# Kernel optimization log

Measured on AMD Instinct MI355X. Metric: run time of the kernel, lower is better.

The kernel has to match this reference:

```python
import jax, jax.numpy as jnp
import numpy as np

D_MODEL = 1024
N_HEADS = 16
D_K = D_MODEL // N_HEADS
D_FF = 4096
EPS = 1e-5


def setup_inputs() -> dict:
    key = jax.random.key(0)
    ks = jax.random.split(key, 16)
    s = 0.02
    d, f = D_MODEL, D_FF
    return {
        'ebd_x': jax.random.normal(ks[0], (2, 2048, d), jnp.float32),
        'Wq': jax.random.normal(ks[1], (d, d), jnp.float32) * s,
        'bq': jnp.zeros((d,), jnp.float32),
        'Wk': jax.random.normal(ks[2], (d, d), jnp.float32) * s,
        'bk': jnp.zeros((d,), jnp.float32),
        'Wv': jax.random.normal(ks[3], (d, d), jnp.float32) * s,
        'bv': jnp.zeros((d,), jnp.float32),
        'Wo': jax.random.normal(ks[4], (d, d), jnp.float32) * s,
        'bo': jnp.zeros((d,), jnp.float32),
        'W1': jax.random.normal(ks[5], (d, f), jnp.float32) * s,
        'b1': jnp.zeros((f,), jnp.float32),
        'W2': jax.random.normal(ks[6], (f, d), jnp.float32) * s,
        'b2': jnp.zeros((d,), jnp.float32),
        'g1': jnp.ones((d,), jnp.float32),
        'beta1': jnp.zeros((d,), jnp.float32),
        'g2': jnp.ones((d,), jnp.float32),
        'beta2': jnp.zeros((d,), jnp.float32),
    }


def _layernorm(x, g, b):
    mu = jnp.mean(x, axis=-1, keepdims=True)
    var = jnp.mean(jnp.square(x - mu), axis=-1, keepdims=True)
    return (x - mu) * jax.lax.rsqrt(var + EPS) * g + b


def reference(ebd_x, Wq, bq, Wk, bk, Wv, bv, Wo, bo, W1, b1, W2, b2, g1, beta1, g2, beta2):
    b, L, d = ebd_x.shape
    h, dk = N_HEADS, D_K
    # QKV projections, split heads: (b, h, L, dk)
    q = (ebd_x @ Wq + bq).reshape(b, L, h, dk).transpose(0, 2, 1, 3)
    k = (ebd_x @ Wk + bk).reshape(b, L, h, dk).transpose(0, 2, 1, 3)
    v = (ebd_x @ Wv + bv).reshape(b, L, h, dk).transpose(0, 2, 1, 3)
    scores = jnp.einsum('bhLd,bhld->bhLl', q, k) / jnp.sqrt(jnp.float32(dk))
    attn = jax.nn.softmax(scores, axis=-1)
    attn_v = jnp.einsum('bhLl,bhld->bhLd', attn, v)
    # faithful to source: reshape (b,h,L,dk) -> (b,L,d) WITHOUT transposing back
    attn_v = attn_v.reshape(b, L, d)
    attn_v = attn_v @ Wo + bo
    # dropout is identity in eval mode
    x1 = _layernorm(attn_v + ebd_x, g1, beta1)
    ff = jax.nn.gelu(x1 @ W1 + b1, approximate=False) @ W2 + b2
    return _layernorm(ff + x1, g2, beta2)
```

## Files before the change

kernel.cpp:

```cpp
#include <hip/hip_runtime.h>
#include <hip/hip_bf16.h>
#include <math.h>

typedef __bf16 bhalf;
typedef __bf16 bhalf8 __attribute__((ext_vector_type(8)));
typedef float  floatx4 __attribute__((ext_vector_type(4)));
typedef float  floatx8 __attribute__((ext_vector_type(8)));
typedef unsigned short ushort_t;
typedef unsigned short ushort8 __attribute__((ext_vector_type(8)));

#define MFMA16(a, b, c) __builtin_amdgcn_mfma_f32_16x16x32_bf16((a), (b), (c), 0, 0, 0)

__device__ __forceinline__ void gload_lds16(const bhalf* g, bhalf* l)
{
    __builtin_amdgcn_global_load_lds((const __attribute__((address_space(1))) void*)g,
                                     (__attribute__((address_space(3))) void*)l, 16, 0, 0);
}

enum { EPI_PLAIN = 0, EPI_RES = 1, EPI_GELU = 2, EPI_QKV = 3 };

__global__ __launch_bounds__(256) void detect_dtype(const ushort_t* __restrict__ x,
                                                    int* __restrict__ flag)
{
    __shared__ int tot;
    if (threadIdx.x == 0) tot = 0;
    __syncthreads();
    int cnt = 0;
#pragma unroll
    for (int it = 0; it < 8; ++it) {
        const ushort8 u = *(const ushort8*)(x + ((size_t)(it * 256 + threadIdx.x)) * 8);
#pragma unroll
        for (int j = 0; j < 8; j += 2) {
            const int e = (u[j] >> 7) & 0xFF;
            if (e >= 0x90) ++cnt;
        }
    }
    atomicAdd(&tot, cnt);
    __syncthreads();
    if (threadIdx.x == 0) flag[0] = (tot > 64) ? 1 : 0;
}

__global__ __launch_bounds__(256) void norm_x(const void* __restrict__ s,
                                              bhalf* __restrict__ d,
                                              const int* __restrict__ flag)
{
    const int i = (blockIdx.x * 256 + threadIdx.x) * 8;
    if (*flag) {
        const floatx8 v = *(const floatx8*)((const float*)s + i);
        bhalf8 o;
#pragma unroll
        for (int j = 0; j < 8; ++j) o[j] = (bhalf)v[j];
        *(bhalf8*)(d + i) = o;
    } else {
        *(ushort8*)((ushort_t*)d + i) = *(const ushort8*)((const ushort_t*)s + i);
    }
}

struct Cvt { const void* s; bhalf* d; int n; };
struct CvtArr { Cvt t[10]; };

__global__ __launch_bounds__(256) void norm_vec(CvtArr a, const int* __restrict__ flag)
{
    const Cvt c = a.t[blockIdx.y];
    const int i = (blockIdx.x * 256 + threadIdx.x) * 8;
    if (i >= c.n) return;
    if (*flag) {
        const floatx8 v = *(const floatx8*)((const float*)c.s + i);
        bhalf8 o;
#pragma unroll
        for (int j = 0; j < 8; ++j) o[j] = (bhalf)v[j];
        *(bhalf8*)(c.d + i) = o;
    } else {
        *(ushort8*)((ushort_t*)c.d + i) = *(const ushort8*)((const ushort_t*)c.s + i);
    }
}

struct TDesc { const void* src; bhalf* dst; int R, C; };
struct TDescArr { TDesc t[6]; };

__global__ __launch_bounds__(256) void transpose_all(TDescArr a, const int* __restrict__ flag)
{
    __shared__ bhalf sm[32][33];
    const int id = blockIdx.x;
    TDesc d;
    int rem;
    if (id < 4096)      { d = a.t[id >> 10]; rem = id & 1023; }
    else if (id < 8192) { d = a.t[4];        rem = id - 4096; }
    else                { d = a.t[5];        rem = id - 8192; }
    const int txc = d.C >> 5;
    const int bx = (rem % txc) * 32;
    const int by = (rem / txc) * 32;
    const int tx = threadIdx.x & 31;
    const int ty = threadIdx.x >> 5;
    if (*flag) {
        const float* fin = (const float*)d.src;
#pragma unroll
        for (int i = 0; i < 4; ++i)
            sm[ty + i * 8][tx] = (bhalf)fin[(size_t)(by + ty + i * 8) * d.C + bx + tx];
    } else {
        const bhalf* bin = (const bhalf*)d.src;
#pragma unroll
        for (int i = 0; i < 4; ++i)
            sm[ty + i * 8][tx] = bin[(size_t)(by + ty + i * 8) * d.C + bx + tx];
    }
    __syncthreads();
#pragma unroll
    for (int i = 0; i < 4; ++i)
        d.dst[(size_t)(bx + ty + i * 8) * d.R + by + tx] = sm[tx][ty + i * 8];
}

__global__ __launch_bounds__(256) void vt_transpose(const bhalf* __restrict__ Vw,
                                                    bhalf* __restrict__ Vt)
{
    __shared__ bhalf sm[32][33];
    const int bh = blockIdx.z;
    const int b = bh >> 4, h = bh & 15;
    const int tb = blockIdx.y * 32;
    const int db = blockIdx.x * 32;
    const int tx = threadIdx.x & 31;
    const int ty = threadIdx.x >> 5;
#pragma unroll
    for (int i = 0; i < 4; ++i)
        sm[ty + i * 8][tx] = Vw[(size_t)(b * 2048 + tb + ty + i * 8) * 1024 + h * 64 + db + tx];
    __syncthreads();
#pragma unroll
    for (int i = 0; i < 4; ++i)
        Vt[(size_t)(bh * 64 + db + ty + i * 8) * 2048 + tb + tx] = sm[tx][ty + i * 8];
}

template <int EPI, int TN>
__global__ __launch_bounds__(256) void gemm128(
    const bhalf* __restrict__ A, int lda,
    const bhalf* __restrict__ BT, int ldb,
    const bhalf* __restrict__ bias,
    const bhalf* __restrict__ resid,
    bhalf* __restrict__ C, int ldc, int K,
    bhalf* __restrict__ Ck, bhalf* __restrict__ Cv)
{
    __shared__ __align__(16) bhalf As[128 * 64];
    __shared__ __align__(16) bhalf Bs[TN * 64];

    const int tid  = threadIdx.x;
    const int lane = tid & 63;
    const int w    = tid >> 6;
    const int l15  = lane & 15;
    const int q    = lane >> 4;
    constexpr int MT = (TN == 128) ? 4 : 2;
    const int wm   = (TN == 128) ? (w >> 1) * 64 : w * 32;
    const int wn   = (TN == 128) ? (w & 1) * 64 : 0;
    const int n0   = blockIdx.x * TN;
    const int m0   = blockIdx.y * 128;

    const int r8 = lane >> 3;
    const int c8 = lane & 7;
    const int gc = (c8 ^ r8) << 3;

    floatx4 acc[MT][4];
#pragma unroll
    for (int i = 0; i < MT; ++i)
#pragma unroll
        for (int j = 0; j < 4; ++j) acc[i][j] = (floatx4){0.f, 0.f, 0.f, 0.f};

    for (int k0 = 0; k0 < K; k0 += 64) {
        __syncthreads();
#pragma unroll
        for (int i = 0; i < 4; ++i) {
            const int rb = w * 32 + i * 8;
            gload_lds16(A + (size_t)(m0 + rb + r8) * lda + k0 + gc, &As[rb * 64] + lane * 8);
        }
        if constexpr (TN == 128) {
#pragma unroll
            for (int i = 0; i < 4; ++i) {
                const int rb = w * 32 + i * 8;
                gload_lds16(BT + (size_t)(n0 + rb + r8) * ldb + k0 + gc, &Bs[rb * 64] + lane * 8);
            }
        } else {
#pragma unroll
            for (int i = 0; i < 2; ++i) {
                const int rb = w * 16 + i * 8;
                gload_lds16(BT + (size_t)(n0 + rb + r8) * ldb + k0 + gc, &Bs[rb * 64] + lane * 8);
            }
        }
        __syncthreads();
#pragma unroll
        for (int s = 0; s < 2; ++s) {
            const int pc = (((s * 4 + q) ^ (l15 & 7)) << 3);
            bhalf8 af[MT], bf[4];
#pragma unroll
            for (int mt = 0; mt < MT; ++mt)
                af[mt] = *(const bhalf8*)&As[(wm + mt * 16 + l15) * 64 + pc];
#pragma unroll
            for (int nt = 0; nt < 4; ++nt)
                bf[nt] = *(const bhalf8*)&Bs[(wn + nt * 16 + l15) * 64 + pc];
#pragma unroll
            for (int mt = 0; mt < MT; ++mt)
#pragma unroll
                for (int nt = 0; nt < 4; ++nt)
                    acc[mt][nt] = MFMA16(af[mt], bf[nt], acc[mt][nt]);
        }
    }

#pragma unroll
    for (int mt = 0; mt < MT; ++mt)
#pragma unroll
        for (int nt = 0; nt < 4; ++nt) {
            const int col = n0 + wn + nt * 16 + l15;
            const float bv = (float)bias[col];
#pragma unroll
            for (int r = 0; r < 4; ++r) {
                const int row = m0 + wm + mt * 16 + q * 4 + r;
                float v = acc[mt][nt][r] + bv;
                if constexpr (EPI == EPI_PLAIN) {
                    C[(size_t)row * ldc + col] = (bhalf)v;
                } else if constexpr (EPI == EPI_RES) {
                    v += (float)resid[(size_t)row * ldc + col];
                    C[(size_t)row * ldc + col] = (bhalf)v;
                } else if constexpr (EPI == EPI_GELU) {
                    v = 0.5f * v * (1.f + erff(v * 0.70710678118654752f));
                    C[(size_t)row * ldc + col] = (bhalf)v;
                } else {
                    if (col < 1024)       C [(size_t)row * 1024 + col]        = (bhalf)v;
                    else if (col < 2048)  Ck[(size_t)row * 1024 + col - 1024] = (bhalf)v;
                    else                  Cv[(size_t)row * 1024 + col - 2048] = (bhalf)v;
                }
            }
        }
}

__global__ __launch_bounds__(256) void flash_attn(
    const bhalf* __restrict__ Q, const bhalf* __restrict__ Km,
    const bhalf* __restrict__ Vt, bhalf* __restrict__ ctx)
{
    __shared__ __align__(16) bhalf Ks[2][64 * 64];
    __shared__ __align__(16) bhalf Vs[2][64 * 64];

    const int tid  = threadIdx.x;
    const int lane = tid & 63;
    const int wq   = tid >> 6;
    const int l15  = lane & 15;
    const int q    = lane >> 4;
    const int bh   = blockIdx.x & 31;
    const int l0   = (blockIdx.x >> 5) * 64;
    const int b    = bh >> 4, h = bh & 15;
    const float SC = 0.125f * 1.44269504f;

    const bhalf* qp = Q + ((size_t)(b * 2048 + l0 + wq * 16 + l15)) * 1024 + h * 64 + q * 8;
    const bhalf8 aQ0 = *(const bhalf8*)qp;
    const bhalf8 aQ1 = *(const bhalf8*)(qp + 32);

    float ps = 0.f;
    floatx4 o[4];
#pragma unroll
    for (int ot = 0; ot < 4; ++ot) o[ot] = (floatx4){0.f, 0.f, 0.f, 0.f};

    const int r8 = lane >> 3;
    const int c8 = lane & 7;
    const bhalf* kbase = Km + ((size_t)(b * 2048)) * 1024 + h * 64;
    const bhalf* vbase = Vt + ((size_t)(bh * 64)) * 2048;

    auto stage = [&](int buf, int kt) {
#pragma unroll
        for (int i = 0; i < 2; ++i) {
            const int rb = wq * 16 + i * 8;
            const int fk = (((rb >> 3) << 1) ^ r8) & 7;
            gload_lds16(kbase + (size_t)(kt + rb + r8) * 1024 + ((c8 ^ fk) << 3),
                        &Ks[buf][rb * 64] + lane * 8);
            gload_lds16(vbase + (size_t)(rb + r8) * 2048 + kt + ((c8 ^ r8) << 3),
                        &Vs[buf][rb * 64] + lane * 8);
        }
    };

    stage(0, 0);
    int cur = 0;
    for (int kt = 0; kt < 2048; kt += 64) {
        __syncthreads();
        if (kt + 64 < 2048) stage(cur ^ 1, kt + 64);

        floatx4 s[4];
#pragma unroll
        for (int nt = 0; nt < 4; ++nt) {
            const int row = (nt >> 1) * 32 + (nt & 1) * 4 + ((l15 >> 2) << 3) + (l15 & 3);
            const int f = (((row >> 3) << 1) ^ row) & 7;
            const bhalf8 k0 = *(const bhalf8*)&Ks[cur][row * 64 + ((q ^ f) << 3)];
            const bhalf8 k1 = *(const bhalf8*)&Ks[cur][row * 64 + (((4 + q) ^ f) << 3)];
            floatx4 z = (floatx4){0.f, 0.f, 0.f, 0.f};
            z = MFMA16(k0, aQ0, z);
            s[nt] = MFMA16(k1, aQ1, z);
        }

        bhalf8 pa[2];
#pragma unroll
        for (int nt = 0; nt < 4; ++nt)
#pragma unroll
            for (int r = 0; r < 4; ++r) {
                const float pv = __builtin_amdgcn_exp2f(fmaf(s[nt][r], SC, -8.f));
                ps += pv;
                pa[nt >> 1][(nt & 1) * 4 + r] = (bhalf)pv;
            }

#pragma unroll
        for (int kc = 0; kc < 2; ++kc)
#pragma unroll
            for (int ot = 0; ot < 4; ++ot) {
                const bhalf8 bV = *(const bhalf8*)&Vs[cur][(ot * 16 + l15) * 64 + (((kc * 4 + q) ^ (l15 & 7)) << 3)];
                o[ot] = MFMA16(pa[kc], bV, o[ot]);
            }
        cur ^= 1;
    }

    ps += __shfl_xor(ps, 16);
    ps += __shfl_xor(ps, 32);
    const float invq = 1.f / ps;
    float inv[4];
#pragma unroll
    for (int r = 0; r < 4; ++r)
        inv[r] = __shfl(invq, (lane & 48) | (q * 4 + r));

#pragma unroll
    for (int ot = 0; ot < 4; ++ot)
#pragma unroll
        for (int r = 0; r < 4; ++r) {
            const int l = l0 + wq * 16 + q * 4 + r;
            const int kk = ot * 16 + l15;
            const int R = h * 128 + (l >> 4);
            const int Cc = (l & 15) * 64 + kk;
            ctx[((size_t)(b * 2048 + R)) * 1024 + Cc] = (bhalf)(o[ot][r] * inv[r]);
        }
}

__global__ __launch_bounds__(256) void ln_kernel(
    const bhalf* __restrict__ X, const bhalf* __restrict__ g,
    const bhalf* __restrict__ be, void* __restrict__ out, const int* __restrict__ flag)
{
    __shared__ float red[4][2];
    const int tid = threadIdx.x;
    const int wid = tid >> 6;
    const int rid = tid >> 7;
    const int lt  = tid & 127;
    const int row = blockIdx.x * 2 + rid;
    const int col = lt * 8;
    const bhalf8 xv = *(const bhalf8*)(X + (size_t)row * 1024 + col);
    float v[8], s1 = 0.f, s2 = 0.f;
#pragma unroll
    for (int i = 0; i < 8; ++i) {
        v[i] = (float)xv[i];
        s1 += v[i];
        s2 += v[i] * v[i];
    }
#pragma unroll
    for (int off = 1; off < 64; off <<= 1) {
        s1 += __shfl_xor(s1, off);
        s2 += __shfl_xor(s2, off);
    }
    if ((tid & 63) == 0) { red[wid][0] = s1; red[wid][1] = s2; }
    __syncthreads();
    const float t1 = red[rid * 2][0] + red[rid * 2 + 1][0];
    const float t2 = red[rid * 2][1] + red[rid * 2 + 1][1];
    const float mu = t1 * (1.f / 1024.f);
    const float rs = rsqrtf(t2 * (1.f / 1024.f) - mu * mu + 1e-5f);
    const bool f32 = flag && (*flag != 0);
    if (f32) {
        floatx8 ov;
#pragma unroll
        for (int i = 0; i < 8; ++i)
            ov[i] = ((v[i] - mu) * rs) * (float)g[col + i] + (float)be[col + i];
        *(floatx8*)((float*)out + (size_t)row * 1024 + col) = ov;
    } else {
        bhalf8 ov;
#pragma unroll
        for (int i = 0; i < 8; ++i)
            ov[i] = (bhalf)(((v[i] - mu) * rs) * (float)g[col + i] + (float)be[col + i]);
        *(bhalf8*)((bhalf*)out + (size_t)row * 1024 + col) = ov;
    }
}

extern "C" void kernel_launch(void* const* d_in, const int* in_sizes, int n_in,
                              void* d_out, int out_size, void* d_ws, size_t ws_size,
                              hipStream_t stream)
{
    (void)in_sizes; (void)n_in; (void)out_size; (void)ws_size;

    char* p = (char*)d_ws;
    const size_t MB = 1024 * 1024;
    int*   flag  = (int*)p;
    bhalf* vecs  = (bhalf*)(p + 128 * 1024);
    bhalf* Qw    = (bhalf*)(p + 1 * MB);
    bhalf* Kw    = (bhalf*)(p + 9 * MB);
    bhalf* Vw    = (bhalf*)(p + 17 * MB);
    bhalf* Vt    = (bhalf*)(p + 25 * MB);
    bhalf* x_n   = (bhalf*)(p + 33 * MB);
    bhalf* WqkvT = (bhalf*)(p + 41 * MB);
    bhalf* WoT   = (bhalf*)(p + 47 * MB);
    bhalf* W1T   = (bhalf*)(p + 49 * MB);
    bhalf* W2T   = (bhalf*)(p + 57 * MB);
    bhalf* ctx   = Vw;
    bhalf* ff1   = (bhalf*)(p + 17 * MB);
    bhalf* ln1   = Qw;
    bhalf* x1    = Kw;
    bhalf* ff2   = Qw;

    bhalf* bqkv  = vecs;
    bhalf* bo_n  = vecs + 1 * 4096;
    bhalf* b1_n  = vecs + 2 * 4096;
    bhalf* b2_n  = vecs + 3 * 4096;
    bhalf* g1_n  = vecs + 4 * 4096;
    bhalf* be1_n = vecs + 5 * 4096;
    bhalf* g2_n  = vecs + 6 * 4096;
    bhalf* be2_n = vecs + 7 * 4096;

    const dim3 blk(256);

    detect_dtype<<<1, blk, 0, stream>>>((const ushort_t*)d_in[0], flag);

    norm_x<<<2048, blk, 0, stream>>>(d_in[0], x_n, flag);
    CvtArr arr;
    arr.t[0] = {d_in[2],  bqkv,        1024};
    arr.t[1] = {d_in[4],  bqkv + 1024, 1024};
    arr.t[2] = {d_in[6],  bqkv + 2048, 1024};
    arr.t[3] = {d_in[8],  bo_n,        1024};
    arr.t[4] = {d_in[10], b1_n,        4096};
    arr.t[5] = {d_in[12], b2_n,        1024};
    arr.t[6] = {d_in[13], g1_n,        1024};
    arr.t[7] = {d_in[14], be1_n,       1024};
    arr.t[8] = {d_in[15], g2_n,        1024};
    arr.t[9] = {d_in[16], be2_n,       1024};
    norm_vec<<<dim3(2, 10), blk, 0, stream>>>(arr, flag);

    TDescArr td;
    td.t[0] = {d_in[1],  WqkvT,               1024, 1024};
    td.t[1] = {d_in[3],  WqkvT + 1024 * 1024, 1024, 1024};
    td.t[2] = {d_in[5],  WqkvT + 2048 * 1024, 1024, 1024};
    td.t[3] = {d_in[7],  WoT,                 1024, 1024};
    td.t[4] = {d_in[9],  W1T,                 1024, 4096};
    td.t[5] = {d_in[11], W2T,                 4096, 1024};
    transpose_all<<<12288, blk, 0, stream>>>(td, flag);

    gemm128<EPI_QKV, 128><<<dim3(24, 32), blk, 0, stream>>>(
        x_n, 1024, WqkvT, 1024, bqkv, nullptr, Qw, 1024, 1024, Kw, Vw);

    vt_transpose<<<dim3(2, 64, 32), blk, 0, stream>>>(Vw, Vt);

    flash_attn<<<1024, blk, 0, stream>>>(Qw, Kw, Vt, ctx);

    gemm128<EPI_RES, 64><<<dim3(16, 32), blk, 0, stream>>>(
        ctx, 1024, WoT, 1024, bo_n, x_n, ln1, 1024, 1024, nullptr, nullptr);
    ln_kernel<<<2048, blk, 0, stream>>>(ln1, g1_n, be1_n, x1, nullptr);

    gemm128<EPI_GELU, 128><<<dim3(32, 32), blk, 0, stream>>>(
        x1, 1024, W1T, 1024, b1_n, nullptr, ff1, 4096, 1024, nullptr, nullptr);
    gemm128<EPI_RES, 64><<<dim3(16, 32), blk, 0, stream>>>(
        ff1, 4096, W2T, 4096, b2_n, x1, ff2, 1024, 4096, nullptr, nullptr);
    ln_kernel<<<2048, blk, 0, stream>>>(ff2, g2_n, be2_n, d_out, flag);
}
```

Before: 381.8 us.

## Add 256x256-tile GEMM with XCD-aware block mapping for QKV and FF1

Introduces a 512-thread GEMM kernel with 256x256 output tiles, double-buffered 128KB dynamic LDS loaded via global_load_lds with XOR swizzle. Block IDs are remapped across the 8 XCDs. The kernel is used for the QKV projection and the GELU FFN up-projection, replacing the 128-tile kernel. Larger tiles raise arithmetic intensity and operand reuse, but the grid shrinks to 192/256 blocks, which risks poor occupancy and load balance on 256 CUs.

```diff
diff --git a/kernel.cpp b/kernel.cpp
--- a/kernel.cpp
+++ b/kernel.cpp
@@ -222,6 +222,109 @@
                     if (col < 1024)       C [(size_t)row * 1024 + col]        = (bhalf)v;
                     else if (col < 2048)  Ck[(size_t)row * 1024 + col - 1024] = (bhalf)v;
                     else                  Cv[(size_t)row * 1024 + col - 2048] = (bhalf)v;
+                }
+            }
+        }
+}
+
+template <int EPI>
+__global__ __launch_bounds__(512, 2) void gemm256(
+    const bhalf* __restrict__ A, int lda,
+    const bhalf* __restrict__ BT, int ldb,
+    const bhalf* __restrict__ bias,
+    bhalf* __restrict__ C, int ldc, int K, int nbx,
+    bhalf* __restrict__ Ck, bhalf* __restrict__ Cv)
+{
+    extern __shared__ __align__(16) bhalf sm[];
+
+    const int tid  = threadIdx.x;
+    const int lane = tid & 63;
+    const int w    = tid >> 6;
+    const int l15  = lane & 15;
+    const int q    = lane >> 4;
+    const int wm   = (w >> 2) * 128;
+    const int wn   = (w & 3) * 64;
+    const int w8   = w * 8;
+
+    const int nwg = gridDim.x;
+    const int cpx = nwg >> 3;
+    const int id  = (blockIdx.x & 7) * cpx + (blockIdx.x >> 3);
+    const int bx  = id % nbx;
+    const int by  = id / nbx;
+    const int n0  = bx * 256;
+    const int m0  = by * 256;
+
+    const int r8 = lane >> 3;
+    const int c8 = lane & 7;
+    const int gc = (c8 ^ r8) << 3;
+
+    floatx4 acc[8][4];
+#pragma unroll
+    for (int i = 0; i < 8; ++i)
+#pragma unroll
+        for (int j = 0; j < 4; ++j) acc[i][j] = (floatx4){0.f, 0.f, 0.f, 0.f};
+
+    auto stage = [&](int buf, int k0) {
+        bhalf* as = sm + buf * 16384;
+        bhalf* bs = sm + 32768 + buf * 16384;
+#pragma unroll
+        for (int i = 0; i < 4; ++i) {
+            const int rb = i * 64 + w8;
+            gload_lds16(A  + (size_t)(m0 + rb + r8) * lda + k0 + gc, as + rb * 64 + lane * 8);
+            gload_lds16(BT + (size_t)(n0 + rb + r8) * ldb + k0 + gc, bs + rb * 64 + lane * 8);
+        }
+    };
+
+    stage(0, 0);
+    const int NT = K >> 6;
+    for (int t = 0; t < NT; ++t) {
+        const int cur = t & 1;
+        const bhalf* as = sm + cur * 16384;
+        const bhalf* bs = sm + 32768 + cur * 16384;
+        __syncthreads();
+        if (t + 1 < NT) stage(cur ^ 1, (t + 1) << 6);
+
+#pragma unroll
+        for (int ks = 0; ks < 2; ++ks) {
+            const int pc = ((ks * 4 + q) ^ (l15 & 7)) << 3;
+            bhalf8 bf[4];
+#pragma unroll
+            for (int nt = 0; nt < 4; ++nt)
+                bf[nt] = *(const bhalf8*)&bs[(wn + nt * 16 + l15) * 64 + pc];
+#pragma unroll
+            for (int mh = 0; mh < 2; ++mh) {
+                bhalf8 af[4];
+#pragma unroll
+                for (int mt = 0; mt < 4; ++mt)
+                    af[mt] = *(const bhalf8*)&as[(wm + mh * 64 + mt * 16 + l15) * 64 + pc];
+#pragma unroll
+                for (int mt = 0; mt < 4; ++mt)
+#pragma unroll
+                    for (int nt = 0; nt < 4; ++nt)
+                        acc[mh * 4 + mt][nt] = MFMA16(af[mt], bf[nt], acc[mh * 4 + mt][nt]);
+            }
+        }
+    }
+
+#pragma unroll
+    for (int j = 0; j < 8; ++j)
+#pragma unroll
+        for (int nt = 0; nt < 4; ++nt) {
+            const int col = n0 + wn + nt * 16 + l15;
+            const float bv = (float)bias[col];
+#pragma unroll
+            for (int r = 0; r < 4; ++r) {
+                const int row = m0 + wm + (j >> 2) * 64 + (j & 3) * 16 + q * 4 + r;
+                float v = acc[j][nt][r] + bv;
+                if constexpr (EPI == EPI_GELU) {
+                    v = 0.5f * v * (1.f + erff(v * 0.70710678118654752f));
+                    C[(size_t)row * ldc + col] = (bhalf)v;
+                } else if constexpr (EPI == EPI_QKV) {
+                    if (col < 1024)       C [(size_t)row * 1024 + col]        = (bhalf)v;
+                    else if (col < 2048)  Ck[(size_t)row * 1024 + col - 1024] = (bhalf)v;
+                    else                  Cv[(size_t)row * 1024 + col - 2048] = (bhalf)v;
+                } else {
+                    C[(size_t)row * ldc + col] = (bhalf)v;
                 }
             }
         }
@@ -408,7 +511,17 @@
     bhalf* g2_n  = vecs + 6 * 4096;
     bhalf* be2_n = vecs + 7 * 4096;
 
+    static bool attr_done = false;
+    if (!attr_done) {
+        hipFuncSetAttribute((const void*)gemm256<EPI_QKV>,
+                            hipFuncAttributeMaxDynamicSharedMemorySize, 131072);
+        hipFuncSetAttribute((const void*)gemm256<EPI_GELU>,
+                            hipFuncAttributeMaxDynamicSharedMemorySize, 131072);
+        attr_done = true;
+    }
+
     const dim3 blk(256);
+    const dim3 blk512(512);
 
     detect_dtype<<<1, blk, 0, stream>>>((const ushort_t*)d_in[0], flag);
 
@@ -435,8 +548,8 @@
     td.t[5] = {d_in[11], W2T,                 4096, 1024};
     transpose_all<<<12288, blk, 0, stream>>>(td, flag);
 
-    gemm128<EPI_QKV, 128><<<dim3(24, 32), blk, 0, stream>>>(
-        x_n, 1024, WqkvT, 1024, bqkv, nullptr, Qw, 1024, 1024, Kw, Vw);
+    gemm256<EPI_QKV><<<192, blk512, 131072, stream>>>(
+        x_n, 1024, WqkvT, 1024, bqkv, Qw, 1024, 1024, 12, Kw, Vw);
 
     vt_transpose<<<dim3(2, 64, 32), blk, 0, stream>>>(Vw, Vt);
 
@@ -446,8 +559,8 @@
         ctx, 1024, WoT, 1024, bo_n, x_n, ln1, 1024, 1024, nullptr, nullptr);
     ln_kernel<<<2048, blk, 0, stream>>>(ln1, g1_n, be1_n, x1, nullptr);
 
-    gemm128<EPI_GELU, 128><<<dim3(32, 32), blk, 0, stream>>>(
-        x1, 1024, W1T, 1024, b1_n, nullptr, ff1, 4096, 1024, nullptr, nullptr);
+    gemm256<EPI_GELU><<<256, blk512, 131072, stream>>>(
+        x1, 1024, W1T, 1024, b1_n, ff1, 4096, 1024, 16, nullptr, nullptr);
     gemm128<EPI_RES, 64><<<dim3(16, 32), blk, 0, stream>>>(
         ff1, 4096, W2T, 4096, b2_n, x1, ff2, 1024, 4096, nullptr, nullptr);
     ln_kernel<<<2048, blk, 0, stream>>>(ff2, g2_n, be2_n, d_out, flag);
```

New measurement: 369.9 us. 3.1% less time.

## Double-buffer GEMM LDS tiles, unify 128x64 tiles, remap blocks across XCDs

Applied to the files above, without the earlier changes.

The GEMM kernel now uses double-buffered LDS, prefetching the next K tile with global_load_lds while MFMAs consume the current one. This removes one barrier per iteration. All GEMMs now use a single 128x64 tile shape on a 1D grid. Block IDs are remapped so that consecutive tiles land on the same XCD (blockIdx mod 8 grouping), which is meant to improve L2 reuse. The 64-wide N tile lowers per-block arithmetic intensity for the QKV and W1 GEMMs and doubles the LDS footprint, which could hurt occupancy.

```diff
diff --git a/kernel.cpp b/kernel.cpp
--- a/kernel.cpp
+++ b/kernel.cpp
@@ -128,72 +128,73 @@
         Vt[(size_t)(bh * 64 + db + ty + i * 8) * 2048 + tb + tx] = sm[tx][ty + i * 8];
 }
 
-template <int EPI, int TN>
+template <int EPI>
 __global__ __launch_bounds__(256) void gemm128(
     const bhalf* __restrict__ A, int lda,
     const bhalf* __restrict__ BT, int ldb,
     const bhalf* __restrict__ bias,
     const bhalf* __restrict__ resid,
-    bhalf* __restrict__ C, int ldc, int K,
+    bhalf* __restrict__ C, int ldc, int K, int nbx,
     bhalf* __restrict__ Ck, bhalf* __restrict__ Cv)
 {
-    __shared__ __align__(16) bhalf As[128 * 64];
-    __shared__ __align__(16) bhalf Bs[TN * 64];
+    __shared__ __align__(16) bhalf As[2][128 * 64];
+    __shared__ __align__(16) bhalf Bs[2][64 * 64];
 
     const int tid  = threadIdx.x;
     const int lane = tid & 63;
     const int w    = tid >> 6;
     const int l15  = lane & 15;
     const int q    = lane >> 4;
-    constexpr int MT = (TN == 128) ? 4 : 2;
-    const int wm   = (TN == 128) ? (w >> 1) * 64 : w * 32;
-    const int wn   = (TN == 128) ? (w & 1) * 64 : 0;
-    const int n0   = blockIdx.x * TN;
-    const int m0   = blockIdx.y * 128;
+    const int wm   = w * 32;
+
+    const int nwg = gridDim.x;
+    const int cpx = nwg >> 3;
+    const int id  = (blockIdx.x & 7) * cpx + (blockIdx.x >> 3);
+    const int n0  = (id % nbx) * 64;
+    const int m0  = (id / nbx) * 128;
 
     const int r8 = lane >> 3;
     const int c8 = lane & 7;
     const int gc = (c8 ^ r8) << 3;
 
-    floatx4 acc[MT][4];
-#pragma unroll
-    for (int i = 0; i < MT; ++i)
+    floatx4 acc[2][4];
+#pragma unroll
+    for (int i = 0; i < 2; ++i)
 #pragma unroll
         for (int j = 0; j < 4; ++j) acc[i][j] = (floatx4){0.f, 0.f, 0.f, 0.f};
 
-    for (int k0 = 0; k0 < K; k0 += 64) {
-        __syncthreads();
+    auto stage = [&](int buf, int k0) {
 #pragma unroll
         for (int i = 0; i < 4; ++i) {
             const int rb = w * 32 + i * 8;
-            gload_lds16(A + (size_t)(m0 + rb + r8) * lda + k0 + gc, &As[rb * 64] + lane * 8);
-        }
-        if constexpr (TN == 128) {
-#pragma unroll
-            for (int i = 0; i < 4; ++i) {
-                const int rb = w * 32 + i * 8;
-                gload_lds16(BT + (size_t)(n0 + rb + r8) * ldb + k0 + gc, &Bs[rb * 64] + lane * 8);
-            }
-        } else {
-#pragma unroll
-            for (int i = 0; i < 2; ++i) {
-                const int rb = w * 16 + i * 8;
-                gload_lds16(BT + (size_t)(n0 + rb + r8) * ldb + k0 + gc, &Bs[rb * 64] + lane * 8);
-            }
-        }
+            gload_lds16(A + (size_t)(m0 + rb + r8) * lda + k0 + gc, &As[buf][rb * 64] + lane * 8);
+        }
+#pragma unroll
+        for (int i = 0; i < 2; ++i) {
+            const int rb = w * 16 + i * 8;
+            gload_lds16(BT + (size_t)(n0 + rb + r8) * ldb + k0 + gc, &Bs[buf][rb * 64] + lane * 8);
+        }
+    };
+
+    stage(0, 0);
+    const int NT = K >> 6;
+    for (int t = 0; t < NT; ++t) {
+        const int cur = t & 1;
         __syncthreads();
+        if (t + 1 < NT) stage(cur ^ 1, (t + 1) << 6);
+
 #pragma unroll
         for (int s = 0; s < 2; ++s) {
             const int pc = (((s * 4 + q) ^ (l15 & 7)) << 3);
-            bhalf8 af[MT], bf[4];
-#pragma unroll
-            for (int mt = 0; mt < MT; ++mt)
-                af[mt] = *(const bhalf8*)&As[(wm + mt * 16 + l15) * 64 + pc];
+            bhalf8 af[2], bf[4];
+#pragma unroll
+            for (int mt = 0; mt < 2; ++mt)
+                af[mt] = *(const bhalf8*)&As[cur][(wm + mt * 16 + l15) * 64 + pc];
 #pragma unroll
             for (int nt = 0; nt < 4; ++nt)
-                bf[nt] = *(const bhalf8*)&Bs[(wn + nt * 16 + l15) * 64 + pc];
-#pragma unroll
-            for (int mt = 0; mt < MT; ++mt)
+                bf[nt] = *(const bhalf8*)&Bs[cur][(nt * 16 + l15) * 64 + pc];
+#pragma unroll
+            for (int mt = 0; mt < 2; ++mt)
 #pragma unroll
                 for (int nt = 0; nt < 4; ++nt)
                     acc[mt][nt] = MFMA16(af[mt], bf[nt], acc[mt][nt]);
@@ -201,27 +202,27 @@
     }
 
 #pragma unroll
-    for (int mt = 0; mt < MT; ++mt)
+    for (int mt = 0; mt < 2; ++mt)
 #pragma unroll
         for (int nt = 0; nt < 4; ++nt) {
-            const int col = n0 + wn + nt * 16 + l15;
+            const int col = n0 + nt * 16 + l15;
             const float bv = (float)bias[col];
 #pragma unroll
             for (int r = 0; r < 4; ++r) {
                 const int row = m0 + wm + mt * 16 + q * 4 + r;
                 float v = acc[mt][nt][r] + bv;
-                if constexpr (EPI == EPI_PLAIN) {
-                    C[(size_t)row * ldc + col] = (bhalf)v;
-                } else if constexpr (EPI == EPI_RES) {
+                if constexpr (EPI == EPI_RES) {
                     v += (float)resid[(size_t)row * ldc + col];
                     C[(size_t)row * ldc + col] = (bhalf)v;
                 } else if constexpr (EPI == EPI_GELU) {
                     v = 0.5f * v * (1.f + erff(v * 0.70710678118654752f));
                     C[(size_t)row * ldc + col] = (bhalf)v;
-                } else {
+                } else if constexpr (EPI == EPI_QKV) {
                     if (col < 1024)       C [(size_t)row * 1024 + col]        = (bhalf)v;
                     else if (col < 2048)  Ck[(size_t)row * 1024 + col - 1024] = (bhalf)v;
                     else                  Cv[(size_t)row * 1024 + col - 2048] = (bhalf)v;
+                } else {
+                    C[(size_t)row * ldc + col] = (bhalf)v;
                 }
             }
         }
@@ -435,20 +436,20 @@
     td.t[5] = {d_in[11], W2T,                 4096, 1024};
     transpose_all<<<12288, blk, 0, stream>>>(td, flag);
 
-    gemm128<EPI_QKV, 128><<<dim3(24, 32), blk, 0, stream>>>(
-        x_n, 1024, WqkvT, 1024, bqkv, nullptr, Qw, 1024, 1024, Kw, Vw);
+    gemm128<EPI_QKV><<<1536, blk, 0, stream>>>(
+        x_n, 1024, WqkvT, 1024, bqkv, nullptr, Qw, 1024, 1024, 48, Kw, Vw);
 
     vt_transpose<<<dim3(2, 64, 32), blk, 0, stream>>>(Vw, Vt);
 
     flash_attn<<<1024, blk, 0, stream>>>(Qw, Kw, Vt, ctx);
 
-    gemm128<EPI_RES, 64><<<dim3(16, 32), blk, 0, stream>>>(
-        ctx, 1024, WoT, 1024, bo_n, x_n, ln1, 1024, 1024, nullptr, nullptr);
+    gemm128<EPI_RES><<<512, blk, 0, stream>>>(
+        ctx, 1024, WoT, 1024, bo_n, x_n, ln1, 1024, 1024, 16, nullptr, nullptr);
     ln_kernel<<<2048, blk, 0, stream>>>(ln1, g1_n, be1_n, x1, nullptr);
 
-    gemm128<EPI_GELU, 128><<<dim3(32, 32), blk, 0, stream>>>(
-        x1, 1024, W1T, 1024, b1_n, nullptr, ff1, 4096, 1024, nullptr, nullptr);
-    gemm128<EPI_RES, 64><<<dim3(16, 32), blk, 0, stream>>>(
-        ff1, 4096, W2T, 4096, b2_n, x1, ff2, 1024, 4096, nullptr, nullptr);
+    gemm128<EPI_GELU><<<2048, blk, 0, stream>>>(
+        x1, 1024, W1T, 1024, b1_n, nullptr, ff1, 4096, 1024, 64, nullptr, nullptr);
+    gemm128<EPI_RES><<<512, blk, 0, stream>>>(
+        ff1, 4096, W2T, 4096, b2_n, x1, ff2, 1024, 4096, 16, nullptr, nullptr);
     ln_kernel<<<2048, blk, 0, stream>>>(ff2, g2_n, be2_n, d_out, flag);
 }
```

Measured after the change: 380.2 us. No clear change (-0.4%).

## Double-buffer GEMM LDS tiles and remap workgroups across XCDs

Applied to the files above, without the earlier changes.

The GEMM kernel now keeps two LDS buffers per operand and issues the global-to-LDS loads for the next K tile before computing the current one, so load latency overlaps with MFMA work. The launch grid is flattened to 1D and workgroup IDs are permuted so that neighbouring tiles land on the same XCD, which should improve L2 reuse of A/B panels. This doubles LDS usage per block, which may reduce occupancy. The loop also assumes an even number of K tiles.

```diff
diff --git a/kernel.cpp b/kernel.cpp
--- a/kernel.cpp
+++ b/kernel.cpp
@@ -134,22 +134,26 @@
     const bhalf* __restrict__ BT, int ldb,
     const bhalf* __restrict__ bias,
     const bhalf* __restrict__ resid,
-    bhalf* __restrict__ C, int ldc, int K,
+    bhalf* __restrict__ C, int ldc, int K, int nbx,
     bhalf* __restrict__ Ck, bhalf* __restrict__ Cv)
 {
-    __shared__ __align__(16) bhalf As[128 * 64];
-    __shared__ __align__(16) bhalf Bs[TN * 64];
+    constexpr int MT = (TN == 128) ? 4 : 2;
+    __shared__ __align__(16) bhalf As[2][128 * 64];
+    __shared__ __align__(16) bhalf Bs[2][TN * 64];
 
     const int tid  = threadIdx.x;
     const int lane = tid & 63;
     const int w    = tid >> 6;
     const int l15  = lane & 15;
     const int q    = lane >> 4;
-    constexpr int MT = (TN == 128) ? 4 : 2;
     const int wm   = (TN == 128) ? (w >> 1) * 64 : w * 32;
     const int wn   = (TN == 128) ? (w & 1) * 64 : 0;
-    const int n0   = blockIdx.x * TN;
-    const int m0   = blockIdx.y * 128;
+
+    const int nwg = gridDim.x;
+    const int cpx = nwg >> 3;
+    const int id  = (blockIdx.x & 7) * cpx + (blockIdx.x >> 3);
+    const int n0  = (id % nbx) * TN;
+    const int m0  = (id / nbx) * 128;
 
     const int r8 = lane >> 3;
     const int c8 = lane & 7;
@@ -161,43 +165,58 @@
 #pragma unroll
         for (int j = 0; j < 4; ++j) acc[i][j] = (floatx4){0.f, 0.f, 0.f, 0.f};
 
-    for (int k0 = 0; k0 < K; k0 += 64) {
-        __syncthreads();
+    const bhalf* Ab = A  + (size_t)(m0 + r8) * lda + gc;
+    const bhalf* Bb = BT + (size_t)(n0 + r8) * ldb + gc;
+
+    auto stage = [&](int buf, int k0) {
 #pragma unroll
         for (int i = 0; i < 4; ++i) {
             const int rb = w * 32 + i * 8;
-            gload_lds16(A + (size_t)(m0 + rb + r8) * lda + k0 + gc, &As[rb * 64] + lane * 8);
+            gload_lds16(Ab + (size_t)rb * lda + k0, &As[buf][rb * 64] + lane * 8);
         }
         if constexpr (TN == 128) {
 #pragma unroll
             for (int i = 0; i < 4; ++i) {
                 const int rb = w * 32 + i * 8;
-                gload_lds16(BT + (size_t)(n0 + rb + r8) * ldb + k0 + gc, &Bs[rb * 64] + lane * 8);
+                gload_lds16(Bb + (size_t)rb * ldb + k0, &Bs[buf][rb * 64] + lane * 8);
             }
         } else {
 #pragma unroll
             for (int i = 0; i < 2; ++i) {
                 const int rb = w * 16 + i * 8;
-                gload_lds16(BT + (size_t)(n0 + rb + r8) * ldb + k0 + gc, &Bs[rb * 64] + lane * 8);
+                gload_lds16(Bb + (size_t)rb * ldb + k0, &Bs[buf][rb * 64] + lane * 8);
             }
         }
-        __syncthreads();
+    };
+
+    auto compute = [&](int buf) {
 #pragma unroll
         for (int s = 0; s < 2; ++s) {
             const int pc = (((s * 4 + q) ^ (l15 & 7)) << 3);
             bhalf8 af[MT], bf[4];
 #pragma unroll
             for (int mt = 0; mt < MT; ++mt)
-                af[mt] = *(const bhalf8*)&As[(wm + mt * 16 + l15) * 64 + pc];
+                af[mt] = *(const bhalf8*)&As[buf][(wm + mt * 16 + l15) * 64 + pc];
 #pragma unroll
             for (int nt = 0; nt < 4; ++nt)
-                bf[nt] = *(const bhalf8*)&Bs[(wn + nt * 16 + l15) * 64 + pc];
+                bf[nt] = *(const bhalf8*)&Bs[buf][(wn + nt * 16 + l15) * 64 + pc];
 #pragma unroll
             for (int mt = 0; mt < MT; ++mt)
 #pragma unroll
                 for (int nt = 0; nt < 4; ++nt)
                     acc[mt][nt] = MFMA16(af[mt], bf[nt], acc[mt][nt]);
         }
+    };
+
+    stage(0, 0);
+    const int NT = K >> 6;
+    for (int t = 0; t < NT; t += 2) {
+        __syncthreads();
+        stage(1, (t + 1) << 6);
+        compute(0);
+        __syncthreads();
+        if (t + 2 < NT) stage(0, (t + 2) << 6);
+        compute(1);
     }
 
 #pragma unroll
@@ -210,18 +229,18 @@
             for (int r = 0; r < 4; ++r) {
                 const int row = m0 + wm + mt * 16 + q * 4 + r;
                 float v = acc[mt][nt][r] + bv;
-                if constexpr (EPI == EPI_PLAIN) {
-                    C[(size_t)row * ldc + col] = (bhalf)v;
-                } else if constexpr (EPI == EPI_RES) {
+                if constexpr (EPI == EPI_RES) {
                     v += (float)resid[(size_t)row * ldc + col];
                     C[(size_t)row * ldc + col] = (bhalf)v;
                 } else if constexpr (EPI == EPI_GELU) {
                     v = 0.5f * v * (1.f + erff(v * 0.70710678118654752f));
                     C[(size_t)row * ldc + col] = (bhalf)v;
-                } else {
+                } else if constexpr (EPI == EPI_QKV) {
                     if (col < 1024)       C [(size_t)row * 1024 + col]        = (bhalf)v;
                     else if (col < 2048)  Ck[(size_t)row * 1024 + col - 1024] = (bhalf)v;
                     else                  Cv[(size_t)row * 1024 + col - 2048] = (bhalf)v;
+                } else {
+                    C[(size_t)row * ldc + col] = (bhalf)v;
                 }
             }
         }
@@ -435,20 +454,20 @@
     td.t[5] = {d_in[11], W2T,                 4096, 1024};
     transpose_all<<<12288, blk, 0, stream>>>(td, flag);
 
-    gemm128<EPI_QKV, 128><<<dim3(24, 32), blk, 0, stream>>>(
-        x_n, 1024, WqkvT, 1024, bqkv, nullptr, Qw, 1024, 1024, Kw, Vw);
+    gemm128<EPI_QKV, 128><<<768, blk, 0, stream>>>(
+        x_n, 1024, WqkvT, 1024, bqkv, nullptr, Qw, 1024, 1024, 24, Kw, Vw);
 
     vt_transpose<<<dim3(2, 64, 32), blk, 0, stream>>>(Vw, Vt);
 
     flash_attn<<<1024, blk, 0, stream>>>(Qw, Kw, Vt, ctx);
 
-    gemm128<EPI_RES, 64><<<dim3(16, 32), blk, 0, stream>>>(
-        ctx, 1024, WoT, 1024, bo_n, x_n, ln1, 1024, 1024, nullptr, nullptr);
+    gemm128<EPI_RES, 64><<<512, blk, 0, stream>>>(
+        ctx, 1024, WoT, 1024, bo_n, x_n, ln1, 1024, 1024, 16, nullptr, nullptr);
     ln_kernel<<<2048, blk, 0, stream>>>(ln1, g1_n, be1_n, x1, nullptr);
 
-    gemm128<EPI_GELU, 128><<<dim3(32, 32), blk, 0, stream>>>(
-        x1, 1024, W1T, 1024, b1_n, nullptr, ff1, 4096, 1024, nullptr, nullptr);
-    gemm128<EPI_RES, 64><<<dim3(16, 32), blk, 0, stream>>>(
-        ff1, 4096, W2T, 4096, b2_n, x1, ff2, 1024, 4096, nullptr, nullptr);
+    gemm128<EPI_GELU, 128><<<1024, blk, 0, stream>>>(
+        x1, 1024, W1T, 1024, b1_n, nullptr, ff1, 4096, 1024, 32, nullptr, nullptr);
+    gemm128<EPI_RES, 64><<<512, blk, 0, stream>>>(
+        ff1, 4096, W2T, 4096, b2_n, x1, ff2, 1024, 4096, 16, nullptr, nullptr);
     ln_kernel<<<2048, blk, 0, stream>>>(ff2, g2_n, be2_n, d_out, flag);
 }
```

Result: slower. 392.6 us (+2.8%).
